# Kernel tuning notes

Hardware: AMD Instinct MI355X
Metric: run time of the kernel (lower is better)

The kernel has to match this reference:

```python
import jax, jax.numpy as jnp
import numpy as np

DIM = 1024
NUM_HEADS = 16
HEAD_DIM = DIM // NUM_HEADS
BATCH = 2
SEQ = 2048


def setup_inputs() -> dict:
    key = jax.random.key(0)
    ks = jax.random.split(key, 9)
    s = 1.0 / np.sqrt(DIM)  # torch Linear default init scale
    x = jax.random.normal(ks[0], (BATCH, SEQ, DIM), dtype=jnp.float32)
    Wq = jax.random.uniform(ks[1], (DIM, DIM), jnp.float32, -s, s)
    bq = jax.random.uniform(ks[2], (DIM,), jnp.float32, -s, s)
    Wk = jax.random.uniform(ks[3], (DIM, DIM), jnp.float32, -s, s)
    bk = jax.random.uniform(ks[4], (DIM,), jnp.float32, -s, s)
    Wv = jax.random.uniform(ks[5], (DIM, DIM), jnp.float32, -s, s)
    bv = jax.random.uniform(ks[6], (DIM,), jnp.float32, -s, s)
    Wo = jax.random.uniform(ks[7], (DIM, DIM), jnp.float32, -s, s)
    bo = jax.random.uniform(ks[8], (DIM,), jnp.float32, -s, s)
    return {"x": x, "Wq": Wq, "bq": bq, "Wk": Wk, "bk": bk,
            "Wv": Wv, "bv": bv, "Wo": Wo, "bo": bo, "enable_causal": 1}


def reference(x, Wq, bq, Wk, bk, Wv, bv, Wo, bo, enable_causal):
    B, S, D = x.shape
    H, Hd = NUM_HEADS, HEAD_DIM
    # projections (torch Linear: x @ W.T + b; W here stored as [out,in])
    q = (x @ Wq.T + bq).reshape(B, S, H, Hd).transpose(0, 2, 1, 3)  # [B,H,S,Hd]
    k = (x @ Wk.T + bk).reshape(B, S, H, Hd).transpose(0, 2, 1, 3)
    v = (x @ Wv.T + bv).reshape(B, S, H, Hd).transpose(0, 2, 1, 3)
    scores = jnp.einsum('bhqd,bhkd->bhqk', q, k) / np.sqrt(Hd)  # [B,H,S,S]
    if enable_causal:
        causal = jnp.triu(jnp.ones((S, S), dtype=bool), k=1)
        scores = jnp.where(causal, -jnp.inf, scores)
    attn = jax.nn.softmax(scores, axis=-1)
    # dropout p=0.0 -> identity (eval-mode math)
    out = jnp.einsum('bhqk,bhkd->bhqd', attn, v)  # [B,H,S,Hd]
    out = out.transpose(0, 2, 1, 3).reshape(B, S, D)
    return out @ Wo.T + bo
```

## Files before the change

### kernel.cpp

```cpp
#include <hip/hip_runtime.h>
#include <hip/hip_bf16.h>
#include <stdint.h>

typedef unsigned short u16;
typedef short bf16x8 __attribute__((ext_vector_type(8)));
typedef float f32x4 __attribute__((ext_vector_type(4)));

#define S_LEN   2048
#define D_MODEL 1024
#define NH      16
#define M_TOK   4096
#define LOG2E   1.4426950408889634f

__device__ __forceinline__ u16 f2b(float f) {
  union { float f; unsigned int u; } v; v.f = f;
  unsigned int r = v.u + 0x7FFFu + ((v.u >> 16) & 1u);
  return (u16)(r >> 16);
}

__device__ __forceinline__ void load_lds16(const void* g, void* l) {
  __builtin_amdgcn_global_load_lds(
      (const __attribute__((address_space(1))) void*)g,
      (__attribute__((address_space(3))) void*)l, 16, 0, 0);
}

__global__ __launch_bounds__(256) void k_convert(
    const float* __restrict__ x,
    const float* __restrict__ wq, const float* __restrict__ wk,
    const float* __restrict__ wv, const float* __restrict__ wo,
    u16* __restrict__ xb, u16* __restrict__ wb)
{
  int t = blockIdx.x * 256 + threadIdx.x;
  long e = (long)t * 8;
  const float* src; u16* dst;
  if (e < (long)M_TOK * D_MODEL) { src = x + e; dst = xb + e; }
  else {
    long we = e - (long)M_TOK * D_MODEL;
    int r = (int)(we >> 20);
    long o = we & 1048575;
    const float* ws = (r == 0) ? wq : (r == 1) ? wk : (r == 2) ? wv : wo;
    src = ws + o; dst = wb + ((long)r << 20) + o;
  }
  float4 f0 = *(const float4*)src;
  float4 f1 = *(const float4*)(src + 4);
  u16 u[8];
  u[0] = f2b(f0.x); u[1] = f2b(f0.y); u[2] = f2b(f0.z); u[3] = f2b(f0.w);
  u[4] = f2b(f1.x); u[5] = f2b(f1.y); u[6] = f2b(f1.z); u[7] = f2b(f1.w);
  *(uint4*)dst = *(const uint4*)u;
}

__device__ __forceinline__ void gemm_mainloop(
    const u16* __restrict__ At, const u16* __restrict__ Bt,
    u16* As, u16* Bs, f32x4 acc[4][4])
{
  const int tid  = threadIdx.x;
  const int lane = tid & 63;
  const int w    = tid >> 6;
  const int wr = w >> 1, wc = w & 1;
  const f32x4 fz = {0.f, 0.f, 0.f, 0.f};
  #pragma unroll
  for (int i = 0; i < 4; ++i)
    #pragma unroll
    for (int j = 0; j < 4; ++j) acc[i][j] = fz;

  const int srow = lane >> 3;
  const int sc   = lane & 7;

  for (int k0 = 0; k0 < D_MODEL; k0 += 64) {
    #pragma unroll
    for (int i = 0; i < 4; ++i) {
      int seg = i * 4 + w;
      int row = seg * 8 + srow;
      load_lds16(At + (long)row * D_MODEL + k0 + sc * 8, (char*)As + seg * 1024);
      load_lds16(Bt + (long)row * D_MODEL + k0 + sc * 8, (char*)Bs + seg * 1024);
    }
    __syncthreads();
    #pragma unroll
    for (int kc = 0; kc < 2; ++kc) {
      bf16x8 af[4], bfv[4];
      #pragma unroll
      for (int mi = 0; mi < 4; ++mi) {
        int row = wr * 64 + mi * 16 + (lane & 15);
        af[mi] = *(const bf16x8*)(As + row * 64 + kc * 32 + (lane >> 4) * 8);
      }
      #pragma unroll
      for (int ni = 0; ni < 4; ++ni) {
        int row = wc * 64 + ni * 16 + (lane & 15);
        bfv[ni] = *(const bf16x8*)(Bs + row * 64 + kc * 32 + (lane >> 4) * 8);
      }
      #pragma unroll
      for (int mi = 0; mi < 4; ++mi)
        #pragma unroll
        for (int ni = 0; ni < 4; ++ni)
          acc[mi][ni] = __builtin_amdgcn_mfma_f32_16x16x32_bf16(
              af[mi], bfv[ni], acc[mi][ni], 0, 0, 0);
    }
    __syncthreads();
  }
}

__global__ __launch_bounds__(256) void k_gemm_qkv(
    const u16* __restrict__ xb, const u16* __restrict__ wb,
    const float* __restrict__ bq, const float* __restrict__ bk,
    const float* __restrict__ bv,
    u16* __restrict__ q, u16* __restrict__ k, u16* __restrict__ v)
{
  __shared__ u16 As[128 * 64];
  __shared__ u16 Bs[128 * 64];
  const int m0   = blockIdx.x * 128;
  const int by   = blockIdx.y;
  const int proj = by >> 3;
  const int n0   = (by & 7) * 128;
  f32x4 acc[4][4];
  gemm_mainloop(xb + (long)m0 * D_MODEL,
                wb + (long)proj * 1048576 + (long)n0 * D_MODEL, As, Bs, acc);

  const int lane = threadIdx.x & 63;
  const int w    = threadIdx.x >> 6;
  const int wr = w >> 1, wc = w & 1;
  const float* bias = (proj == 0) ? bq : (proj == 1) ? bk : bv;
  u16* dst = (proj == 0) ? q : (proj == 1) ? k : v;
  const float sc = (proj == 0) ? 0.125f * LOG2E : 1.0f;
  #pragma unroll
  for (int mi = 0; mi < 4; ++mi)
    #pragma unroll
    for (int ni = 0; ni < 4; ++ni) {
      int n = n0 + wc * 64 + ni * 16 + (lane & 15);
      float bval = bias[n];
      int h = n >> 6, d = n & 63;
      #pragma unroll
      for (int r = 0; r < 4; ++r) {
        int m = m0 + wr * 64 + mi * 16 + (lane >> 4) * 4 + r;
        int b = m >> 11, s = m & 2047;
        float val = (acc[mi][ni][r] + bval) * sc;
        dst[(((long)(b * NH + h) * S_LEN + s) << 6) + d] = f2b(val);
      }
    }
}

__global__ __launch_bounds__(256) void k_transpose_v(
    const u16* __restrict__ v, u16* __restrict__ vt)
{
  __shared__ u16 t[64][65];
  const int bh = blockIdx.y;
  const int s0 = blockIdx.x * 64;
  const int tid = threadIdx.x;
  const int r = tid >> 2, cg = tid & 3;
  const u16* src = v + ((long)bh * S_LEN + s0 + r) * 64 + cg * 16;
  uint4 a = *(const uint4*)src;
  uint4 b = *(const uint4*)(src + 8);
  u16 tmp[16];
  *(uint4*)tmp = a; *(uint4*)(tmp + 8) = b;
  #pragma unroll
  for (int j = 0; j < 16; ++j) t[r][cg * 16 + j] = tmp[j];
  __syncthreads();
  u16 o[16];
  #pragma unroll
  for (int j = 0; j < 16; ++j) o[j] = t[cg * 16 + j][r];
  u16* dst = vt + ((long)bh * 64 + r) * S_LEN + s0 + cg * 16;
  *(uint4*)dst = *(const uint4*)o;
  *(uint4*)(dst + 8) = *(const uint4*)(o + 8);
}

__global__ __launch_bounds__(256) void k_attn(
    const u16* __restrict__ Q, const u16* __restrict__ K,
    const u16* __restrict__ Vt, u16* __restrict__ O,
    const int* __restrict__ causal_flag)
{
  __shared__ u16 Ks[2][64 * 64];
  __shared__ u16 Ps[4][16 * 72];

  const int tid  = threadIdx.x;
  const int lane = tid & 63;
  const int w    = tid >> 6;
  const int bid  = blockIdx.x;
  const int xcd  = bid & 7;
  const int j    = bid >> 3;
  const int bh   = xcd * 4 + (j & 3);
  const int qb   = 31 - (j >> 2);
  const int q0   = qb * 64;
  const int causal = *causal_flag;

  const int l15 = lane & 15;
  const int l4  = lane >> 4;

  const u16* Kbh  = K  + (long)bh * S_LEN * 64;
  const u16* Vtbh = Vt + (long)bh * 64 * S_LEN;
  const f32x4 fz = {0.f, 0.f, 0.f, 0.f};
  const int nt = causal ? (qb + 1) : (S_LEN / 64);

  bf16x8 onesv;
  #pragma unroll
  for (int i = 0; i < 8; ++i) onesv[i] = (short)0x3F80;

  #define STAGE_K(bufp, kv0_)  do {                                          \
    _Pragma("unroll")                                                        \
    for (int i_ = 0; i_ < 2; ++i_) {                                         \
      int base_ = i_ * 256 + w * 64;           \
      int row_  = (base_ >> 3) + (lane >> 3);                                \
      int csrc_ = (lane & 7) ^ (row_ & 7);                                   \
      load_lds16(Kbh + (long)((kv0_) + row_) * 64 + csrc_ * 8,               \
                 (char*)(bufp) + base_ * 16);                                \
    }                                                                        \
  } while (0)

  const u16* Qb = Q + ((long)bh * S_LEN + q0 + w * 16) * 64;
  bf16x8 qf0 = *(const bf16x8*)(Qb + l15 * 64 +      l4 * 8);
  bf16x8 qf1 = *(const bf16x8*)(Qb + l15 * 64 + 32 + l4 * 8);

  f32x4 acc_o[4] = {fz, fz, fz, fz};
  f32x4 acc_l = fz;

  int cur = 0;
  STAGE_K(Ks[0], 0);
  asm volatile("s_waitcnt vmcnt(0)" ::: "memory");
  __builtin_amdgcn_s_barrier();

  #pragma unroll 1
  for (int t = 0; t < nt; ++t) {
    const int kv0 = t * 64;

    bf16x8 vf0[4], vf1[4];
    #pragma unroll
    for (int sub = 0; sub < 4; ++sub) {
      const u16* Vd = Vtbh + (long)(sub * 16 + l15) * S_LEN + kv0;
      vf0[sub] = *(const bf16x8*)(Vd +      l4 * 8);
      vf1[sub] = *(const bf16x8*)(Vd + 32 + l4 * 8);
    }

    if (t + 1 < nt) STAGE_K(Ks[cur ^ 1], kv0 + 64);

    f32x4 acc_s[4] = {fz, fz, fz, fz};
    __builtin_amdgcn_s_setprio(1);
    #pragma unroll
    for (int kc = 0; kc < 2; ++kc) {
      bf16x8 qf = kc ? qf1 : qf0;
      #pragma unroll
      for (int sub = 0; sub < 4; ++sub) {
        int krow = sub * 16 + l15;
        int cs = (kc * 4 + l4) ^ (krow & 7);
        bf16x8 kf = *(const bf16x8*)(Ks[cur] + krow * 64 + cs * 8);
        acc_s[sub] = __builtin_amdgcn_mfma_f32_16x16x32_bf16(qf, kf, acc_s[sub], 0, 0, 0);
      }
    }
    __builtin_amdgcn_s_setprio(0);

    if (causal && t == nt - 1) {
      #pragma unroll
      for (int sub = 0; sub < 4; ++sub) {
        int kvcol = kv0 + sub * 16 + l15;
        #pragma unroll
        for (int r = 0; r < 4; ++r) {
          int qrow = q0 + w * 16 + l4 * 4 + r;
          if (kvcol > qrow) acc_s[sub][r] = -1e30f;
        }
      }
    }

    u16* P = &Ps[w][0];
    #pragma unroll
    for (int sub = 0; sub < 4; ++sub)
      #pragma unroll
      for (int r = 0; r < 4; ++r) {
        float p = exp2f(acc_s[sub][r]);
        __hip_bfloat16 hb = __float2bfloat16(p);
        P[(l4 * 4 + r) * 72 + sub * 16 + l15] = *(u16*)&hb;
      }

    asm volatile("s_waitcnt lgkmcnt(0)" ::: "memory");
    bf16x8 pf0 = *(const bf16x8*)(P + l15 * 72 +      l4 * 8);
    bf16x8 pf1 = *(const bf16x8*)(P + l15 * 72 + 32 + l4 * 8);
    __builtin_amdgcn_s_setprio(1);
    #pragma unroll
    for (int sub = 0; sub < 4; ++sub) {
      acc_o[sub] = __builtin_amdgcn_mfma_f32_16x16x32_bf16(pf0, vf0[sub], acc_o[sub], 0, 0, 0);
      acc_o[sub] = __builtin_amdgcn_mfma_f32_16x16x32_bf16(pf1, vf1[sub], acc_o[sub], 0, 0, 0);
    }
    acc_l = __builtin_amdgcn_mfma_f32_16x16x32_bf16(pf0, onesv, acc_l, 0, 0, 0);
    acc_l = __builtin_amdgcn_mfma_f32_16x16x32_bf16(pf1, onesv, acc_l, 0, 0, 0);
    __builtin_amdgcn_s_setprio(0);

    if (t + 1 < nt) {
      asm volatile("s_waitcnt vmcnt(0)" ::: "memory");
      __builtin_amdgcn_s_barrier();
      cur ^= 1;
    }
  }
  #undef STAGE_K

  const int b = bh >> 4, h = bh & 15;
  #pragma unroll
  for (int sub = 0; sub < 4; ++sub)
    #pragma unroll
    for (int r = 0; r < 4; ++r) {
      int s = q0 + w * 16 + l4 * 4 + r;
      float val = acc_o[sub][r] / acc_l[r];
      O[((long)(b * S_LEN + s)) * D_MODEL + h * 64 + sub * 16 + l15] = f2b(val);
    }
}

__global__ __launch_bounds__(256) void k_gemm_o(
    const u16* __restrict__ ob, const u16* __restrict__ wb,
    const float* __restrict__ bo, float* __restrict__ out)
{
  __shared__ u16 As[128 * 64];
  __shared__ u16 Bs[128 * 64];
  const int m0 = blockIdx.x * 128;
  const int n0 = blockIdx.y * 128;
  f32x4 acc[4][4];
  gemm_mainloop(ob + (long)m0 * D_MODEL,
                wb + 3L * 1048576 + (long)n0 * D_MODEL, As, Bs, acc);
  const int lane = threadIdx.x & 63;
  const int w    = threadIdx.x >> 6;
  const int wr = w >> 1, wc = w & 1;
  #pragma unroll
  for (int mi = 0; mi < 4; ++mi)
    #pragma unroll
    for (int ni = 0; ni < 4; ++ni) {
      int n = n0 + wc * 64 + ni * 16 + (lane & 15);
      float bval = bo[n];
      #pragma unroll
      for (int r = 0; r < 4; ++r) {
        int m = m0 + wr * 64 + mi * 16 + (lane >> 4) * 4 + r;
        out[(long)m * D_MODEL + n] = acc[mi][ni][r] + bval;
      }
    }
}

extern "C" void kernel_launch(void* const* d_in, const int* in_sizes, int n_in,
                              void* d_out, int out_size, void* d_ws, size_t ws_size,
                              hipStream_t stream) {
  const float* x  = (const float*)d_in[0];
  const float* Wq = (const float*)d_in[1];
  const float* bq = (const float*)d_in[2];
  const float* Wk = (const float*)d_in[3];
  const float* bk = (const float*)d_in[4];
  const float* Wv = (const float*)d_in[5];
  const float* bv = (const float*)d_in[6];
  const float* Wo = (const float*)d_in[7];
  const float* bo = (const float*)d_in[8];
  const int* causal = (const int*)d_in[9];
  float* out = (float*)d_out;

  char* ws = (char*)d_ws;
  u16* xb = (u16*)(ws);
  u16* wb = (u16*)(ws + (8L  << 20));
  u16* qb = (u16*)(ws + (16L << 20));
  u16* kb = (u16*)(ws + (24L << 20));
  u16* vb = (u16*)(ws + (32L << 20));
  u16* vt = (u16*)(ws + (40L << 20));
  u16* ob = (u16*)(ws);

  k_convert   <<<4096,          256, 0, stream>>>(x, Wq, Wk, Wv, Wo, xb, wb);
  k_gemm_qkv  <<<dim3(32, 24),  256, 0, stream>>>(xb, wb, bq, bk, bv, qb, kb, vb);
  k_transpose_v<<<dim3(32, 32), 256, 0, stream>>>(vb, vt);
  k_attn      <<<1024,          256, 0, stream>>>(qb, kb, vt, ob, causal);
  k_gemm_o    <<<dim3(32, 8),   256, 0, stream>>>(ob, wb, bo, out);
}
```

Before: 255.2 us.

## Rebalance causal attention block order and streamline exp, addressing, and normalization

```diff
diff --git a/kernel.cpp b/kernel.cpp
--- a/kernel.cpp
+++ b/kernel.cpp
@@ -16,6 +16,12 @@
   union { float f; unsigned int u; } v; v.f = f;
   unsigned int r = v.u + 0x7FFFu + ((v.u >> 16) & 1u);
   return (u16)(r >> 16);
+}
+
+__device__ __forceinline__ float exp2_fast(float x) {
+  float r;
+  asm("v_exp_f32 %0, %1" : "=v"(r) : "v"(x));
+  return r;
 }
 
 __device__ __forceinline__ void load_lds16(const void* g, void* l) {
@@ -176,8 +182,11 @@
   const int bid  = blockIdx.x;
   const int xcd  = bid & 7;
   const int j    = bid >> 3;
-  const int bh   = xcd * 4 + (j & 3);
-  const int qb   = 31 - (j >> 2);
+  const int kk   = j >> 5;
+  const int c    = j & 31;
+  const int bh   = xcd * 4 + kk;
+  const int cc   = (kk & 2) ? ((c + 16) & 31) : c;
+  const int qb   = (kk & 1) ? (31 - cc) : cc;
   const int q0   = qb * 64;
   const int causal = *causal_flag;
 
@@ -193,16 +202,26 @@
   #pragma unroll
   for (int i = 0; i < 8; ++i) onesv[i] = (short)0x3F80;
 
-  #define STAGE_K(bufp, kv0_)  do {                                          \
-    _Pragma("unroll")                                                        \
-    for (int i_ = 0; i_ < 2; ++i_) {                                         \
-      int base_ = i_ * 256 + w * 64;           \
-      int row_  = (base_ >> 3) + (lane >> 3);                                \
-      int csrc_ = (lane & 7) ^ (row_ & 7);                                   \
-      load_lds16(Kbh + (long)((kv0_) + row_) * 64 + csrc_ * 8,               \
-                 (char*)(bufp) + base_ * 16);                                \
-    }                                                                        \
+  const u16 *kg0, *kg1; int lo0, lo1;
+  {
+    int b0 = w * 64;
+    int r0 = (b0 >> 3) + (lane >> 3);
+    int c0 = (lane & 7) ^ (r0 & 7);
+    kg0 = Kbh + r0 * 64 + c0 * 8;  lo0 = b0 * 16;
+    int b1 = 256 + w * 64;
+    int r1 = (b1 >> 3) + (lane >> 3);
+    int c1 = (lane & 7) ^ (r1 & 7);
+    kg1 = Kbh + r1 * 64 + c1 * 8;  lo1 = b1 * 16;
+  }
+  #define STAGE_T(bufp, toff) do {                                   \
+    load_lds16(kg0 + (toff) * 4096, (char*)(bufp) + lo0);            \
+    load_lds16(kg1 + (toff) * 4096, (char*)(bufp) + lo1);            \
   } while (0)
+
+  const u16* Vp0 = Vtbh + (long)( 0 + l15) * S_LEN + l4 * 8;
+  const u16* Vp1 = Vtbh + (long)(16 + l15) * S_LEN + l4 * 8;
+  const u16* Vp2 = Vtbh + (long)(32 + l15) * S_LEN + l4 * 8;
+  const u16* Vp3 = Vtbh + (long)(48 + l15) * S_LEN + l4 * 8;
 
   const u16* Qb = Q + ((long)bh * S_LEN + q0 + w * 16) * 64;
   bf16x8 qf0 = *(const bf16x8*)(Qb + l15 * 64 +      l4 * 8);
@@ -212,23 +231,19 @@
   f32x4 acc_l = fz;
 
   int cur = 0;
-  STAGE_K(Ks[0], 0);
+  STAGE_T(Ks[0], 0);
   asm volatile("s_waitcnt vmcnt(0)" ::: "memory");
   __builtin_amdgcn_s_barrier();
 
   #pragma unroll 1
   for (int t = 0; t < nt; ++t) {
-    const int kv0 = t * 64;
-
     bf16x8 vf0[4], vf1[4];
-    #pragma unroll
-    for (int sub = 0; sub < 4; ++sub) {
-      const u16* Vd = Vtbh + (long)(sub * 16 + l15) * S_LEN + kv0;
-      vf0[sub] = *(const bf16x8*)(Vd +      l4 * 8);
-      vf1[sub] = *(const bf16x8*)(Vd + 32 + l4 * 8);
-    }
-
-    if (t + 1 < nt) STAGE_K(Ks[cur ^ 1], kv0 + 64);
+    vf0[0] = *(const bf16x8*)(Vp0); vf1[0] = *(const bf16x8*)(Vp0 + 32);
+    vf0[1] = *(const bf16x8*)(Vp1); vf1[1] = *(const bf16x8*)(Vp1 + 32);
+    vf0[2] = *(const bf16x8*)(Vp2); vf1[2] = *(const bf16x8*)(Vp2 + 32);
+    vf0[3] = *(const bf16x8*)(Vp3); vf1[3] = *(const bf16x8*)(Vp3 + 32);
+
+    if (t + 1 < nt) STAGE_T(Ks[cur ^ 1], t + 1);
 
     f32x4 acc_s[4] = {fz, fz, fz, fz};
     __builtin_amdgcn_s_setprio(1);
@@ -248,7 +263,7 @@
     if (causal && t == nt - 1) {
       #pragma unroll
       for (int sub = 0; sub < 4; ++sub) {
-        int kvcol = kv0 + sub * 16 + l15;
+        int kvcol = t * 64 + sub * 16 + l15;
         #pragma unroll
         for (int r = 0; r < 4; ++r) {
           int qrow = q0 + w * 16 + l4 * 4 + r;
@@ -262,9 +277,8 @@
     for (int sub = 0; sub < 4; ++sub)
       #pragma unroll
       for (int r = 0; r < 4; ++r) {
-        float p = exp2f(acc_s[sub][r]);
-        __hip_bfloat16 hb = __float2bfloat16(p);
-        P[(l4 * 4 + r) * 72 + sub * 16 + l15] = *(u16*)&hb;
+        float p = exp2_fast(acc_s[sub][r]);
+        P[(l4 * 4 + r) * 72 + sub * 16 + l15] = f2b(p);
       }
 
     asm volatile("s_waitcnt lgkmcnt(0)" ::: "memory");
@@ -285,16 +299,22 @@
       __builtin_amdgcn_s_barrier();
       cur ^= 1;
     }
-  }
-  #undef STAGE_K
+    Vp0 += 64; Vp1 += 64; Vp2 += 64; Vp3 += 64;
+  }
+  #undef STAGE_T
 
   const int b = bh >> 4, h = bh & 15;
+  float rl[4];
+  #pragma unroll
+  for (int r = 0; r < 4; ++r) {
+    asm("v_rcp_f32 %0, %1" : "=v"(rl[r]) : "v"(acc_l[r]));
+  }
   #pragma unroll
   for (int sub = 0; sub < 4; ++sub)
     #pragma unroll
     for (int r = 0; r < 4; ++r) {
       int s = q0 + w * 16 + l4 * 4 + r;
-      float val = acc_o[sub][r] / acc_l[r];
+      float val = acc_o[sub][r] * rl[r];
       O[((long)(b * S_LEN + s)) * D_MODEL + h * 64 + sub * 16 + l15] = f2b(val);
     }
 }
```

New measurement: 251.3 us. About the same (-1.5%).
